# Optimization experiments

Hardware: AMD Instinct MI355X
Metric: run time of the kernel (lower is better)

## Reference

```python
import jax, jax.numpy as jnp
import numpy as np
from jax import lax

DIM = 256
HEADS = 8


def dwconv3x3(x, w, b):
    # x: [B,C,H,W], w: [C,1,3,3] depthwise (groups=C), b: [C]
    y = lax.conv_general_dilated(
        x, w, window_strides=(1, 1), padding='SAME',
        dimension_numbers=('NCHW', 'OIHW', 'NCHW'),
        feature_group_count=x.shape[1])
    return y + b[None, :, None, None]


def conv1x1(x, w, b):
    # x: [B,Cin,H,W], w: [Cout,Cin], b: [Cout]
    return jnp.einsum('oc,bchw->bohw', w, x) + b[None, :, None, None]


def setup_inputs() -> dict:
    key = jax.random.key(0)
    ks = jax.random.split(key, 12)
    s = 0.05
    inp = {
        'x': jax.random.normal(ks[0], (4, DIM, 128, 128), dtype=jnp.float32),
        'q_w': jax.random.normal(ks[1], (DIM, 1, 3, 3), dtype=jnp.float32) * s,
        'q_b': jax.random.normal(ks[2], (DIM,), dtype=jnp.float32) * s,
        'k_w': jax.random.normal(ks[3], (DIM, 1, 3, 3), dtype=jnp.float32) * s,
        'k_b': jax.random.normal(ks[4], (DIM,), dtype=jnp.float32) * s,
        'v_w': jax.random.normal(ks[5], (DIM, 1, 3, 3), dtype=jnp.float32) * s,
        'v_b': jax.random.normal(ks[6], (DIM,), dtype=jnp.float32) * s,
        'out_w': jax.random.normal(ks[7], (DIM, DIM), dtype=jnp.float32) * s,
        'out_b': jax.random.normal(ks[8], (DIM,), dtype=jnp.float32) * s,
        'fusion_w': jax.random.normal(ks[9], (DIM, 2 * DIM), dtype=jnp.float32) * s,
        'fusion_b': jax.random.normal(ks[10], (DIM,), dtype=jnp.float32) * s,
        'temperature': jnp.ones((HEADS, 1, 1), dtype=jnp.float32),
        'gamma': jax.random.normal(ks[11], (1,), dtype=jnp.float32) * 0.1,
    }
    return inp


def reference(x, q_w, q_b, k_w, k_b, v_w, v_b, out_w, out_b,
              fusion_w, fusion_b, temperature, gamma):
    b, c, h, w = x.shape
    ch = c // HEADS  # channels per head (32)
    q = dwconv3x3(x, q_w, q_b).reshape(b, HEADS, ch, h * w)
    k = dwconv3x3(x, k_w, k_b).reshape(b, HEADS, ch, h * w)
    v = dwconv3x3(x, v_w, v_b).reshape(b, HEADS, ch, h * w)
    # channel-wise attention: [b, head, c, c]
    attn = jnp.einsum('bhcn,bhdn->bhcd', q, k) * temperature[None]
    attn = jax.nn.softmax(attn, axis=-1)
    out = jnp.einsum('bhcd,bhdn->bhcn', attn, v).reshape(b, c, h, w)
    out = conv1x1(out, out_w, out_b)
    fused = jnp.concatenate([out * gamma[0], x], axis=1)  # [b, 2c, h, w]
    return conv1x1(fused, fusion_w, fusion_b)
```

## Files before the change

### kernel.cpp

```cpp
#include <hip/hip_runtime.h>

typedef __attribute__((ext_vector_type(8))) short bf16x8;
typedef __attribute__((ext_vector_type(4))) float f32x4;

static __device__ __forceinline__ unsigned short f2bf(float f) {
  unsigned u = __builtin_bit_cast(unsigned, f);
  unsigned r = u + 0x7fffu + ((u >> 16) & 1u);
  return (unsigned short)(r >> 16);
}
static __device__ __forceinline__ unsigned pkbf(float a, float b) {
  return (unsigned)f2bf(a) | ((unsigned)f2bf(b) << 16);
}

#define GLOAD_LDS16(g, l)                                              \
  __builtin_amdgcn_global_load_lds(                                    \
      (const __attribute__((address_space(1))) void*)(g),              \
      (__attribute__((address_space(3))) void*)(l), 16, 0, 0)

struct SmA { float xs[5184]; unsigned short qk[2][32][256]; };
union SmU { SmA a; unsigned short vx[256][72]; };

__global__ __launch_bounds__(256, 3) void k_qkv(
    const float* __restrict__ x,
    const float* __restrict__ q_w, const float* __restrict__ q_b,
    const float* __restrict__ k_w, const float* __restrict__ k_b,
    const float* __restrict__ v_w, const float* __restrict__ v_b,
    unsigned short* __restrict__ bx,
    float* __restrict__ gp)
{
  __shared__ SmU sm;
  const int lin = blockIdx.x + 64 * (blockIdx.y + 8 * blockIdx.z);
  const int nl = ((lin & 7) << 8) | (lin >> 3);
  const int t = nl & 63, h = (nl >> 6) & 7, b = nl >> 9;
  const int tid = threadIdx.x;
  __builtin_assume(tid < 256);
  const int wv = tid >> 6, lane = tid & 63;
  const int w4 = __builtin_amdgcn_readfirstlane(wv);
  const int ty = t >> 3, tx = t & 7;
  const int y0 = ty * 16, x0 = tx * 16;
  const int py = lane >> 2, px0 = (lane & 3) * 4;

  float ra[21], rb[21];
  #pragma unroll
  for (int it = 0; it < 21; ++it) {
    int i = tid + it * 256;
    ra[it] = 0.f; rb[it] = 0.f;
    if (i < 5184) {
      int c = i / 324, r = i - c * 324;
      int yy = r / 18, xx = r - yy * 18;
      int gy = y0 + yy - 1, gx = x0 + xx - 1;
      if ((unsigned)gy < 128u && (unsigned)gx < 128u) {
        const float* p = x + (((size_t)(b * 256 + h * 32 + c)) * 128 + gy) * 128 + gx;
        ra[it] = p[0];
        rb[it] = p[16 * 16384];
      }
    }
  }

  uint2 vpack[2][4], xpack[2][4];
  #pragma unroll
  for (int pass = 0; pass < 2; ++pass) {
    #pragma unroll
    for (int it = 0; it < 21; ++it) {
      int i = tid + it * 256;
      if (i < 5184) sm.a.xs[i] = pass ? rb[it] : ra[it];
    }
    __syncthreads();

    const int cbase = h * 32 + pass * 16;
    float vvf[4][4], xxf[4][4];
    #pragma unroll
    for (int j = 0; j < 4; ++j) {
      const int cl = w4 * 4 + j;
      const int ch = cbase + cl;
      float wq[9], wk[9], wvv[9];
      #pragma unroll
      for (int i2 = 0; i2 < 9; ++i2) {
        wq[i2]  = q_w[ch * 9 + i2];
        wk[i2]  = k_w[ch * 9 + i2];
        wvv[i2] = v_w[ch * 9 + i2];
      }
      const float bq = q_b[ch], bk = k_b[ch], bv = v_b[ch];
      float win[3][6];
      #pragma unroll
      for (int r = 0; r < 3; ++r) {
        const float* xrow = &sm.a.xs[cl * 324 + (py + r) * 18 + px0];
        float2 a01 = *(const float2*)&xrow[0];
        float2 a23 = *(const float2*)&xrow[2];
        float2 a45 = *(const float2*)&xrow[4];
        win[r][0] = a01.x; win[r][1] = a01.y;
        win[r][2] = a23.x; win[r][3] = a23.y;
        win[r][4] = a45.x; win[r][5] = a45.y;
      }
      const int ah = pass * 16 + cl;
      float q4[4], k4[4];
      #pragma unroll
      for (int px = 0; px < 4; ++px) {
        float aq = bq, ak = bk, av = bv;
        #pragma unroll
        for (int r = 0; r < 3; ++r)
          #pragma unroll
          for (int cx = 0; cx < 3; ++cx) {
            float xv = win[r][px + cx];
            aq += wq[r * 3 + cx] * xv;
            ak += wk[r * 3 + cx] * xv;
            av += wvv[r * 3 + cx] * xv;
          }
        q4[px] = aq; k4[px] = ak;
        vvf[j][px] = av;
        xxf[j][px] = win[1][px + 1];
      }
      const int sw = (((lane >> 1) ^ (ah & 7)) << 3) + ((lane & 1) << 2);
      *(uint2*)&sm.a.qk[0][ah][sw] = make_uint2(pkbf(q4[0], q4[1]), pkbf(q4[2], q4[3]));
      *(uint2*)&sm.a.qk[1][ah][sw] = make_uint2(pkbf(k4[0], k4[1]), pkbf(k4[2], k4[3]));
    }
    #pragma unroll
    for (int px = 0; px < 4; ++px) {
      vpack[pass][px] = make_uint2(pkbf(vvf[0][px], vvf[1][px]), pkbf(vvf[2][px], vvf[3][px]));
      xpack[pass][px] = make_uint2(pkbf(xxf[0][px], xxf[1][px]), pkbf(xxf[2][px], xxf[3][px]));
    }
    __syncthreads();
  }

  const int qm = wv >> 1, qn = wv & 1;
  const int lrow = lane & 15, quad = lane >> 4;
  const int rowa = qm * 16 + lrow, rowb = qn * 16 + lrow;
  f32x4 acc = {0.f, 0.f, 0.f, 0.f};
  #pragma unroll
  for (int ks = 0; ks < 8; ++ks) {
    bf16x8 a  = *(const bf16x8*)&sm.a.qk[0][rowa][(((ks * 4 + quad) ^ (rowa & 7)) << 3)];
    bf16x8 bb = *(const bf16x8*)&sm.a.qk[1][rowb][(((ks * 4 + quad) ^ (rowb & 7)) << 3)];
    acc = __builtin_amdgcn_mfma_f32_16x16x32_bf16(a, bb, acc, 0, 0, 0);
  }
  float* gpb = gp + ((size_t)((b * 8 + h) * 64 + t)) * 1024;
  #pragma unroll
  for (int r = 0; r < 4; ++r)
    gpb[(qm * 16 + quad * 4 + r) * 32 + qn * 16 + lrow] = acc[r];

  __syncthreads();

  const int chi = wv >> 1, half = wv & 1;
  #pragma unroll
  for (int pass = 0; pass < 2; ++pass)
    #pragma unroll
    for (int px = 0; px < 4; ++px) {
      int n = py * 16 + px0 + px;
      int key = (n >> 3) & 7;
      int cv = pass * 2 + chi;
      int cx2 = 4 + pass * 2 + chi;
      *(uint2*)&sm.vx[n][((cv ^ key) << 3) + (half << 2)] = vpack[pass][px];
      *(uint2*)&sm.vx[n][((cx2 ^ key) << 3) + (half << 2)] = xpack[pass][px];
    }
  __syncthreads();

  #pragma unroll
  for (int it = 0; it < 8; ++it) {
    int n = it * 32 + (tid >> 3);
    int m = tid & 7;
    int key = (n >> 3) & 7;
    uint4 val = *(const uint4*)&sm.vx[n][((m ^ key) << 3)];
    int pyn = n >> 4, pxn = n & 15;
    int ng = (y0 + pyn) * 128 + x0 + pxn;
    *(uint4*)&bx[((size_t)b * 16384 + ng) * 512 + h * 64 + m * 8] = val;
  }
}

__global__ __launch_bounds__(256) void k_rs_prep(
    const float* __restrict__ gp, const float* __restrict__ temp,
    float* __restrict__ attn,
    const float* __restrict__ out_w, const float* __restrict__ out_b,
    const float* __restrict__ fusion_w, const float* __restrict__ fusion_b,
    const float* __restrict__ gamma,
    float* __restrict__ W1g, float* __restrict__ bias_tot,
    unsigned short* __restrict__ Wcat) {
  const int bi = blockIdx.x;
  const int tid = threadIdx.x;

  if (bi >= 128) {
    const int o = bi - 128;
    const int c = tid;
    const float g = gamma[0];
    float acc = 0.f, bacc = 0.f;
    #pragma unroll 8
    for (int t = 0; t < 256; ++t) {
      float fw = fusion_w[o*512 + t];
      acc  += fw * out_w[t*256 + c];
      bacc += fw * out_b[t];
    }
    W1g[o*256 + c] = g * acc;
    if (c == 0) bias_tot[o] = g * bacc + fusion_b[o];
    unsigned short w2b = f2bf(fusion_w[o*512 + 256 + c]);
    const int col = ((c >> 5) << 6) + 32 + (c & 31);
    for (int b = 0; b < 4; ++b)
      Wcat[((size_t)(b*256 + o))*512 + col] = w2b;
    return;
  }

  const int cs = bi & 3, h = (bi >> 2) & 7, b = bi >> 5;
  const int lc = tid >> 5, d = tid & 31;
  const int c = cs * 8 + lc;
  const float* base = gp + ((size_t)((b*8 + h)*64))*1024 + c*32 + d;
  float s = 0.f;
  #pragma unroll
  for (int g = 0; g < 8; ++g) {
    float p = 0.f;
    #pragma unroll
    for (int i = 0; i < 8; ++i) p += base[(size_t)(g*8 + i)*1024];
    s += p;
  }
  s *= temp[h];
  float m = s;
  #pragma unroll
  for (int off = 16; off; off >>= 1) m = fmaxf(m, __shfl_xor(m, off));
  float e = __expf(s - m);
  float sum = e;
  #pragma unroll
  for (int off = 16; off; off >>= 1) sum += __shfl_xor(sum, off);
  attn[((size_t)((b*8 + h)*32 + c))*32 + d] = e / sum;
}

__global__ __launch_bounds__(256) void k_compose(
    const float* __restrict__ W1g, const float* __restrict__ attn,
    unsigned short* __restrict__ Wcat) {
  const int o = blockIdx.x, b = blockIdx.y;
  const int e = threadIdx.x;
  const int h = e >> 5, d = e & 31;
  const float* ab = attn + ((size_t)((b*8 + h)*32))*32 + d;
  const float* wb = W1g + o*256 + h*32;
  float s = 0.f;
  #pragma unroll
  for (int c2 = 0; c2 < 32; ++c2) s += wb[c2] * ab[c2*32];
  Wcat[((size_t)(b*256 + o))*512 + ((e >> 5) << 6) + (e & 31)] = f2bf(s);
}

__global__ __launch_bounds__(256) void k_gemm(
    const unsigned short* __restrict__ Wcat,
    const unsigned short* __restrict__ bx,
    const float* __restrict__ bias_tot,
    float* __restrict__ out) {
  __shared__ unsigned short Al[2][256][32];
  __shared__ unsigned short Bl[2][64][32];
  const int nt = blockIdx.x, b = blockIdx.y;
  const int tid = threadIdx.x;
  const int wv = tid >> 6, lane = tid & 63;
  const int lrow = lane & 15, quad = lane >> 4;
  const int nbase = nt * 64;
  const unsigned short* Ab = Wcat + (size_t)b * 256 * 512;
  const unsigned short* Bb = bx + ((size_t)b * 16384 + nbase) * 512;
  f32x4 acc[4][4] = {};

  const int srow = tid >> 2;
  const int sq4 = tid & 3;
  const unsigned short* apr = Ab + (size_t)srow * 512 + sq4 * 8;
  const unsigned short* bpr = Bb + (size_t)srow * 512 + sq4 * 8;

  #pragma unroll
  for (int g = 0; g < 4; ++g)
    GLOAD_LDS16(apr + (size_t)g * 64 * 512, &Al[0][wv * 16 + g * 64][0]);
  GLOAD_LDS16(bpr, &Bl[0][wv * 16][0]);
  __syncthreads();

  for (int ks = 0; ks < 16; ++ks) {
    const int cur = ks & 1;
    if (ks < 15) {
      const int k0 = (ks + 1) * 32;
      const int nxt = cur ^ 1;
      #pragma unroll
      for (int g = 0; g < 4; ++g)
        GLOAD_LDS16(apr + (size_t)g * 64 * 512 + k0, &Al[nxt][wv * 16 + g * 64][0]);
      GLOAD_LDS16(bpr + k0, &Bl[nxt][wv * 16][0]);
    }
    bf16x8 af[4], bfv[4];
    #pragma unroll
    for (int i = 0; i < 4; ++i)
      af[i] = *(const bf16x8*)&Al[cur][wv * 64 + i * 16 + lrow][quad * 8];
    #pragma unroll
    for (int j = 0; j < 4; ++j)
      bfv[j] = *(const bf16x8*)&Bl[cur][j * 16 + lrow][quad * 8];
    #pragma unroll
    for (int i = 0; i < 4; ++i)
      #pragma unroll
      for (int j = 0; j < 4; ++j)
        acc[i][j] = __builtin_amdgcn_mfma_f32_16x16x32_bf16(af[i], bfv[j], acc[i][j], 0, 0, 0);
    __syncthreads();
  }

  #pragma unroll
  for (int i = 0; i < 4; ++i) {
    #pragma unroll
    for (int r = 0; r < 4; ++r) {
      const int o = wv*64 + i*16 + quad*4 + r;
      const float bias = bias_tot[o];
      #pragma unroll
      for (int j = 0; j < 4; ++j) {
        const int n = nbase + j*16 + lrow;
        out[((size_t)(b*256 + o))*16384 + n] = acc[i][j][r] + bias;
      }
    }
  }
}

extern "C" void kernel_launch(void* const* d_in, const int* in_sizes, int n_in,
                              void* d_out, int out_size, void* d_ws, size_t ws_size,
                              hipStream_t stream) {
  const float* x        = (const float*)d_in[0];
  const float* q_w      = (const float*)d_in[1];
  const float* q_b      = (const float*)d_in[2];
  const float* k_w      = (const float*)d_in[3];
  const float* k_b      = (const float*)d_in[4];
  const float* v_w      = (const float*)d_in[5];
  const float* v_b      = (const float*)d_in[6];
  const float* out_w    = (const float*)d_in[7];
  const float* out_b    = (const float*)d_in[8];
  const float* fusion_w = (const float*)d_in[9];
  const float* fusion_b = (const float*)d_in[10];
  const float* temp     = (const float*)d_in[11];
  const float* gamma    = (const float*)d_in[12];
  float* out = (float*)d_out;

  char* ws = (char*)d_ws;
  unsigned short* bx   = (unsigned short*)(ws);
  float* gp            = (float*)(ws + 67108864);
  float* attn          = (float*)(ws + 75497472);
  float* W1g           = (float*)(ws + 75628544);
  float* bias_tot      = (float*)(ws + 75890688);
  unsigned short* Wcat = (unsigned short*)(ws + 75891712);

  k_qkv<<<dim3(64, 8, 4), dim3(256), 0, stream>>>(x, q_w, q_b, k_w, k_b, v_w, v_b, bx, gp);
  k_rs_prep<<<dim3(384), dim3(256), 0, stream>>>(gp, temp, attn,
                                                 out_w, out_b, fusion_w, fusion_b,
                                                 gamma, W1g, bias_tot, Wcat);
  k_compose<<<dim3(256, 4), dim3(256), 0, stream>>>(W1g, attn, Wcat);
  k_gemm<<<dim3(256, 4), dim3(256), 0, stream>>>(Wcat, bx, bias_tot, out);
}
```

Measured before the change: 221.1 us.

## Stage halo tiles in per-wave LDS slices and drop block barriers in qkv

Each wave now loads only the halo tiles for its own four channels into registers. It stages them one channel at a time into a private LDS slice of 324 floats, instead of the whole block filling a shared 16-channel buffer. This removes the two block-wide barriers per pass and shrinks the LDS footprint, so launch bounds are raised from 3 to 4 blocks per CU. The trade-off is more register pressure from the 48-float prefetch array under a tighter register budget, with a possible risk of spills.

```diff
diff --git a/kernel.cpp b/kernel.cpp
--- a/kernel.cpp
+++ b/kernel.cpp
@@ -17,10 +17,10 @@
       (const __attribute__((address_space(1))) void*)(g),              \
       (__attribute__((address_space(3))) void*)(l), 16, 0, 0)
 
-struct SmA { float xs[5184]; unsigned short qk[2][32][256]; };
+struct SmA { float xs[4][324]; unsigned short qk[2][32][256]; };
 union SmU { SmA a; unsigned short vx[256][72]; };
 
-__global__ __launch_bounds__(256, 3) void k_qkv(
+__global__ __launch_bounds__(256, 4) void k_qkv(
     const float* __restrict__ x,
     const float* __restrict__ q_w, const float* __restrict__ q_b,
     const float* __restrict__ k_w, const float* __restrict__ k_b,
@@ -40,39 +40,43 @@
   const int y0 = ty * 16, x0 = tx * 16;
   const int py = lane >> 2, px0 = (lane & 3) * 4;
 
-  float ra[21], rb[21];
-  #pragma unroll
-  for (int it = 0; it < 21; ++it) {
-    int i = tid + it * 256;
-    ra[it] = 0.f; rb[it] = 0.f;
-    if (i < 5184) {
-      int c = i / 324, r = i - c * 324;
-      int yy = r / 18, xx = r - yy * 18;
-      int gy = y0 + yy - 1, gx = x0 + xx - 1;
-      if ((unsigned)gy < 128u && (unsigned)gx < 128u) {
-        const float* p = x + (((size_t)(b * 256 + h * 32 + c)) * 128 + gy) * 128 + gx;
-        ra[it] = p[0];
-        rb[it] = p[16 * 16384];
-      }
-    }
-  }
-
+  int goff[6]; bool gok[6];
+  #pragma unroll
+  for (int k = 0; k < 6; ++k) {
+    int r = lane + 64 * k;
+    int yy = r / 18, xx = r - yy * 18;
+    int gy = y0 + yy - 1, gx = x0 + xx - 1;
+    gok[k] = (r < 324) && ((unsigned)gy < 128u) && ((unsigned)gx < 128u);
+    goff[k] = gy * 128 + gx;
+  }
+  const float* cb = x + ((size_t)(b * 256 + h * 32 + w4 * 4)) * 16384;
+  float ha[2][4][6];
+  #pragma unroll
+  for (int pass = 0; pass < 2; ++pass)
+    #pragma unroll
+    for (int j = 0; j < 4; ++j) {
+      const float* p = cb + ((size_t)(pass * 16 + j)) * 16384;
+      #pragma unroll
+      for (int k = 0; k < 6; ++k) {
+        ha[pass][j][k] = 0.f;
+        if (gok[k]) ha[pass][j][k] = p[goff[k]];
+      }
+    }
+
+  float* xw = &sm.a.xs[w4][0];
   uint2 vpack[2][4], xpack[2][4];
   #pragma unroll
   for (int pass = 0; pass < 2; ++pass) {
-    #pragma unroll
-    for (int it = 0; it < 21; ++it) {
-      int i = tid + it * 256;
-      if (i < 5184) sm.a.xs[i] = pass ? rb[it] : ra[it];
-    }
-    __syncthreads();
-
     const int cbase = h * 32 + pass * 16;
     float vvf[4][4], xxf[4][4];
     #pragma unroll
     for (int j = 0; j < 4; ++j) {
-      const int cl = w4 * 4 + j;
-      const int ch = cbase + cl;
+      #pragma unroll
+      for (int k = 0; k < 6; ++k) {
+        int r = lane + 64 * k;
+        if (r < 324) xw[r] = ha[pass][j][k];
+      }
+      const int ch = cbase + w4 * 4 + j;
       float wq[9], wk[9], wvv[9];
       #pragma unroll
       for (int i2 = 0; i2 < 9; ++i2) {
@@ -84,7 +88,7 @@
       float win[3][6];
       #pragma unroll
       for (int r = 0; r < 3; ++r) {
-        const float* xrow = &sm.a.xs[cl * 324 + (py + r) * 18 + px0];
+        const float* xrow = &xw[(py + r) * 18 + px0];
         float2 a01 = *(const float2*)&xrow[0];
         float2 a23 = *(const float2*)&xrow[2];
         float2 a45 = *(const float2*)&xrow[4];
@@ -92,7 +96,7 @@
         win[r][2] = a23.x; win[r][3] = a23.y;
         win[r][4] = a45.x; win[r][5] = a45.y;
       }
-      const int ah = pass * 16 + cl;
+      const int ah = pass * 16 + w4 * 4 + j;
       float q4[4], k4[4];
       #pragma unroll
       for (int px = 0; px < 4; ++px) {
@@ -119,8 +123,8 @@
       vpack[pass][px] = make_uint2(pkbf(vvf[0][px], vvf[1][px]), pkbf(vvf[2][px], vvf[3][px]));
       xpack[pass][px] = make_uint2(pkbf(xxf[0][px], xxf[1][px]), pkbf(xxf[2][px], xxf[3][px]));
     }
-    __syncthreads();
-  }
+  }
+  __syncthreads();
 
   const int qm = wv >> 1, qn = wv & 1;
   const int lrow = lane & 15, quad = lane >> 4;
```

Result: slower. 258.4 us (+16.9%).
